# Optimization experiments

Hardware: AMD Instinct MI355X
Metric: run time of the kernel (lower is better)

## Reference

```python
import jax, jax.numpy as jnp
from jax import lax
import numpy as np

B, T = 64, 1024
N_MELS, ENC, DEC, LSTM, SPK = 80, 256, 128, 512, 256
CTX = ENC + SPK          # encoder_seq feature dim = 512
PRE = 2 * DEC            # prenet fc dims = 256
FILTERS, KS = 32, 31
MAX_R, R = 20, 1         # r buffer initialized to 1
DROP_P = 0.5


def _gru_cell(x, h, w_ih, w_hh, b_ih, b_hh):
    gi = x @ w_ih.T + b_ih
    gh = h @ w_hh.T + b_hh
    i_r, i_z, i_n = jnp.split(gi, 3, axis=-1)
    h_r, h_z, h_n = jnp.split(gh, 3, axis=-1)
    r = jax.nn.sigmoid(i_r + h_r)
    z = jax.nn.sigmoid(i_z + h_z)
    n = jnp.tanh(i_n + r * h_n)
    return (1.0 - z) * n + z * h


def _lstm_cell(x, h, c, w_ih, w_hh, b_ih, b_hh):
    g = x @ w_ih.T + h @ w_hh.T + b_ih + b_hh
    i, f, gg, o = jnp.split(g, 4, axis=-1)
    c2 = jax.nn.sigmoid(f) * c + jax.nn.sigmoid(i) * jnp.tanh(gg)
    h2 = jax.nn.sigmoid(o) * jnp.tanh(c2)
    return h2, c2


def setup_inputs() -> dict:
    key = jax.random.key(0)
    ks = jax.random.split(key, 40)
    n = lambda i, shp: jax.random.normal(ks[i], shp, jnp.float32)
    p = lambda i, shp: jax.random.normal(ks[i], shp, jnp.float32) * 0.05
    return {
        "encoder_seq": n(0, (B, T, CTX)),
        "encoder_seq_proj": n(1, (B, T, DEC)),
        "prenet_in": n(2, (B, N_MELS)),
        "attn_hidden": n(3, (B, DEC)),
        "rnn1_hidden": n(4, (B, LSTM)),
        "rnn2_hidden": n(5, (B, LSTM)),
        "rnn1_cell": n(6, (B, LSTM)),
        "rnn2_cell": n(7, (B, LSTM)),
        "context_vec": n(8, (B, CTX)),
        "chars": jax.random.randint(ks[9], (B, T), 0, 100),
        "t": 0,
        # LSA params (torch layout: Linear weight [out,in])
        "conv_w": p(10, (FILTERS, 1, KS)),
        "conv_b": p(11, (FILTERS,)),
        "L_w": p(12, (DEC, FILTERS)),
        "W_w": p(13, (DEC, DEC)),
        "W_b": p(14, (DEC,)),
        "v_w": p(15, (1, DEC)),
        # PreNet
        "fc1_w": p(16, (PRE, N_MELS)),
        "fc1_b": p(17, (PRE,)),
        "fc2_w": p(18, (PRE, PRE)),
        "fc2_b": p(19, (PRE,)),
        # GRUCell: in = CTX + PRE = 768, hidden = DEC
        "gru_w_ih": p(20, (3 * DEC, CTX + PRE)),
        "gru_w_hh": p(21, (3 * DEC, DEC)),
        "gru_b_ih": p(22, (3 * DEC,)),
        "gru_b_hh": p(23, (3 * DEC,)),
        # rnn_input Linear: CTX + DEC = 640 -> LSTM
        "ri_w": p(24, (LSTM, CTX + DEC)),
        "ri_b": p(25, (LSTM,)),
        # LSTMCells
        "l1_w_ih": p(26, (4 * LSTM, LSTM)),
        "l1_w_hh": p(27, (4 * LSTM, LSTM)),
        "l1_b_ih": p(28, (4 * LSTM,)),
        "l1_b_hh": p(29, (4 * LSTM,)),
        "l2_w_ih": p(30, (4 * LSTM, LSTM)),
        "l2_w_hh": p(31, (4 * LSTM, LSTM)),
        "l2_b_ih": p(32, (4 * LSTM,)),
        "l2_b_hh": p(33, (4 * LSTM,)),
        # output projections
        "mp_w": p(34, (N_MELS * MAX_R, LSTM)),
        "sp_w": p(35, (1, CTX + LSTM)),
        "sp_b": p(36, (1,)),
    }


def reference(encoder_seq, encoder_seq_proj, prenet_in, attn_hidden, rnn1_hidden,
              rnn2_hidden, rnn1_cell, rnn2_cell, context_vec, chars, t,
              conv_w, conv_b, L_w, W_w, W_b, v_w,
              fc1_w, fc1_b, fc2_w, fc2_b,
              gru_w_ih, gru_w_hh, gru_b_ih, gru_b_hh,
              ri_w, ri_b,
              l1_w_ih, l1_w_hh, l1_b_ih, l1_b_hh,
              l2_w_ih, l2_w_hh, l2_b_ih, l2_b_hh,
              mp_w, sp_w, sp_b):
    # PreNet (dropout always on, deterministic keys)
    dk1, dk2 = jax.random.split(jax.random.key(42))
    keep = 1.0 - DROP_P
    h = jax.nn.relu(prenet_in @ fc1_w.T + fc1_b)
    h = h * jax.random.bernoulli(dk1, keep, h.shape).astype(h.dtype) / keep
    h = jax.nn.relu(h @ fc2_w.T + fc2_b)
    prenet_out = h * jax.random.bernoulli(dk2, keep, h.shape).astype(h.dtype) / keep

    # attention GRU
    attn_h = _gru_cell(jnp.concatenate([context_vec, prenet_out], axis=-1),
                       attn_hidden, gru_w_ih, gru_w_hh, gru_b_ih, gru_b_hh)

    # LSA attention at t == 0 (cumulative attention is zeros)
    pq = attn_h @ W_w.T + W_b                              # [B, DEC]
    cumulative = jnp.zeros((B, 1, T), encoder_seq.dtype)
    loc = lax.conv_general_dilated(cumulative, conv_w, (1,), [((KS - 1) // 2,) * 2],
                                   dimension_numbers=("NCH", "OIH", "NCH"))
    loc = loc + conv_b[None, :, None]                      # [B, F, T]
    ploc = jnp.swapaxes(loc, 1, 2) @ L_w.T                 # [B, T, DEC]
    u = (jnp.tanh(pq[:, None, :] + encoder_seq_proj + ploc) @ v_w.T)[..., 0]  # [B, T]
    u = u * (chars != 0).astype(u.dtype)
    scores = jax.nn.softmax(u, axis=1)                     # [B, T]
    context = jnp.einsum("bt,btd->bd", scores, encoder_seq)  # [B, CTX]

    # residual LSTM stack (inference: no zoneout)
    x = jnp.concatenate([context, attn_h], axis=1) @ ri_w.T + ri_b
    h1, c1 = _lstm_cell(x, rnn1_hidden, rnn1_cell, l1_w_ih, l1_w_hh, l1_b_ih, l1_b_hh)
    x = x + h1
    h2, c2 = _lstm_cell(x, rnn2_hidden, rnn2_cell, l2_w_ih, l2_w_hh, l2_b_ih, l2_b_hh)
    x = x + h2

    mels = (x @ mp_w.T).reshape(B, N_MELS, MAX_R)[:, :, :R]  # [B, n_mels, r]
    stop = jax.nn.sigmoid(jnp.concatenate([x, context], axis=1) @ sp_w.T + sp_b)
    return mels, scores[:, None, :], attn_h, h1, h2, c1, c2, context, stop
```

## Files before the change

### kernel.cpp

```cpp
#include <hip/hip_runtime.h>
#include <stdint.h>

#define JAX_PARTITIONABLE 1
#define NB 512

__device__ __forceinline__ float tanh_f(float x) {
  float e = __expf(2.0f * x);
  return 1.0f - 2.0f / (e + 1.0f);
}
__device__ __forceinline__ float sigm(float x) {
  return 1.0f / (1.0f + __expf(-x));
}

__device__ __forceinline__ void stw(float* p, float v) {
  __hip_atomic_store(p, v, __ATOMIC_RELAXED, __HIP_MEMORY_SCOPE_AGENT);
}

__device__ __forceinline__ void tf2x32(unsigned k0, unsigned k1, unsigned x0, unsigned x1,
                                       unsigned &o0, unsigned &o1) {
  unsigned ks0 = k0, ks1 = k1, ks2 = k0 ^ k1 ^ 0x1BD11BDAu;
  x0 += ks0; x1 += ks1;
#define RR(r) { x0 += x1; x1 = (x1 << r) | (x1 >> (32 - r)); x1 ^= x0; }
  RR(13) RR(15) RR(26) RR(6)  x0 += ks1; x1 += ks2 + 1u;
  RR(17) RR(29) RR(16) RR(24) x0 += ks2; x1 += ks0 + 2u;
  RR(13) RR(15) RR(26) RR(6)  x0 += ks0; x1 += ks1 + 3u;
  RR(17) RR(29) RR(16) RR(24) x0 += ks1; x1 += ks2 + 4u;
  RR(13) RR(15) RR(26) RR(6)  x0 += ks2; x1 += ks0 + 5u;
#undef RR
  o0 = x0; o1 = x1;
}

__device__ __forceinline__ float drop_scale(unsigned k0, unsigned k1, unsigned flat) {
#if JAX_PARTITIONABLE
  unsigned o0, o1; tf2x32(k0, k1, 0u, flat, o0, o1);
  unsigned bits = o0 ^ o1;
#else
  unsigned o0, o1, bits;
  if (flat < 8192u) { tf2x32(k0, k1, flat, flat + 8192u, o0, o1); bits = o0; }
  else             { tf2x32(k0, k1, flat - 8192u, flat, o0, o1); bits = o1; }
#endif
  return (bits >> 31) ? 0.0f : 2.0f;
}
__device__ __forceinline__ void get_drop_keys(unsigned &a0, unsigned &a1,
                                              unsigned &b0, unsigned &b1) {
#if JAX_PARTITIONABLE
  tf2x32(0u, 42u, 0u, 0u, a0, a1);
  tf2x32(0u, 42u, 0u, 1u, b0, b1);
#else
  unsigned p0, q0, p1, q1;
  tf2x32(0u, 42u, 0u, 2u, p0, q0);
  tf2x32(0u, 42u, 1u, 3u, p1, q1);
  a0 = p0; a1 = p1; b0 = q0; b1 = q1;
#endif
}

__device__ __forceinline__ void gbar(int* ibase, int phase) {
  __syncthreads();
  if (threadIdx.x == 0) {
    const int s = (int)(blockIdx.x & 15);
    int* sub   = ibase + s * 64;
    int* top   = ibase + 1024;
    int* flags = ibase + 1088;
    int old = __hip_atomic_fetch_add(sub, 1, __ATOMIC_RELAXED, __HIP_MEMORY_SCOPE_AGENT);
    if (old == phase * 32 - 1) {
      int t = __hip_atomic_fetch_add(top, 1, __ATOMIC_RELAXED, __HIP_MEMORY_SCOPE_AGENT);
      if (t == phase * 16 - 1) {
        #pragma unroll
        for (int i = 0; i < 16; i++)
          __hip_atomic_store(flags + i * 64, phase, __ATOMIC_RELAXED, __HIP_MEMORY_SCOPE_AGENT);
      }
    }
    long long guard = 0;
    while (__hip_atomic_load(flags + s * 64, __ATOMIC_RELAXED, __HIP_MEMORY_SCOPE_AGENT) < phase) {
      __builtin_amdgcn_s_sleep(4);
      if (++guard > (1LL << 21)) break;
    }
  }
  __syncthreads();
}

__global__ void k0(int* cnt) {
  for (int i = threadIdx.x; i < 2112; i += 256) cnt[i] = 0;
}

__global__ __launch_bounds__(256, 2) void kM(
    const float* es, const float* esp, const float* prenet_in,
    const float* rnn1_hidden, const float* rnn2_hidden,
    const float* rnn1_cell, const float* rnn2_cell,
    const float* context_vec, const float* attn_hidden, const int* chars,
    const float* conv_b, const float* L_w, const float* W_w, const float* W_b, const float* v_w,
    const float* fc1_w, const float* fc1_b, const float* fc2_w, const float* fc2_b,
    const float* gru_w_ih, const float* gru_w_hh, const float* gru_b_ih, const float* gru_b_hh,
    const float* ri_w, const float* ri_b,
    const float* l1_w_ih, const float* l1_w_hh, const float* l1_b_ih, const float* l1_b_hh,
    const float* l2_w_ih, const float* l2_w_hh, const float* l2_b_ih, const float* l2_b_hh,
    const float* mp_w, const float* sp_w, const float* sp_b,
    float* ws,
    float* mels_o, float* scores_o, float* attn_o, float* h1_o, float* h2_o,
    float* c1_o, float* c2_o, float* ctx_o, float* stop_o) {
  int* ibase = (int*)ws;
  float* pqc     = ws + 2112;
  float* phT     = pqc + 128;
  float* poT     = phT + 16384;
  float* attn_hT = poT + 16384;
  float* u_buf   = attn_hT + 8192;
  float* ctxT    = u_buf + 65536;
  float* xT      = ctxT + 32768;
  float* x2T     = xT + 32768;
  float* x3T     = x2T + 32768;
  float* h1pT    = x3T + 32768;
  float* h2pT    = h1pT + 32768;
  float* cvT     = h2pT + 32768;
  float* ahT0    = cvT + 32768;
  float* c1pT    = ahT0 + 8192;
  float* c2pT    = c1pT + 32768;

  const int g = blockIdx.x, tid = threadIdx.x;
  const int w = tid >> 6, lane = tid & 63;
  __shared__ float sh[16640];

  if (g < 64) {
    for (int i = tid; i < 5120; i += 256) sh[(i / 80) * 81 + (i % 80)] = prenet_in[i];
    __syncthreads();
    unsigned d1k0, d1k1, d2k0, d2k1;
    get_drop_keys(d1k0, d1k1, d2k0, d2k1);
    const int j = g * 4 + w;
    float acc = fc1_b[j];
    const float* wr = fc1_w + j * 80;
    #pragma unroll 8
    for (int k = 0; k < 80; k += 2) {
      float2 wv = *(const float2*)(wr + k);
      acc += sh[lane * 81 + k] * wv.x + sh[lane * 81 + k + 1] * wv.y;
    }
    acc = fmaxf(acc, 0.0f) * drop_scale(d1k0, d1k1, (unsigned)(lane * 256 + j));
    stw(&phT[j * 64 + lane], acc);
  } else if (g < 128) {
    int base = (g - 64) * 512;
    #pragma unroll
    for (int e = 0; e < 2; e++) { int i = base + tid + e * 256; stw(&h1pT[i], rnn1_hidden[(i & 63) * 512 + (i >> 6)]); }
  } else if (g < 192) {
    int base = (g - 128) * 512;
    #pragma unroll
    for (int e = 0; e < 2; e++) { int i = base + tid + e * 256; stw(&h2pT[i], rnn2_hidden[(i & 63) * 512 + (i >> 6)]); }
  } else if (g < 256) {
    int base = (g - 192) * 512;
    #pragma unroll
    for (int e = 0; e < 2; e++) { int i = base + tid + e * 256; stw(&cvT[i], context_vec[(i & 63) * 512 + (i >> 6)]); }
  } else if (g < 272) {
    int base = (g - 256) * 512;
    #pragma unroll
    for (int e = 0; e < 2; e++) { int i = base + tid + e * 256; stw(&ahT0[i], attn_hidden[(i & 63) * 128 + (i >> 6)]); }
  } else if (g < 336) {
    int base = (g - 272) * 512;
    #pragma unroll
    for (int e = 0; e < 2; e++) { int i = base + tid + e * 256; stw(&c1pT[i], rnn1_cell[(i & 63) * 512 + (i >> 6)]); }
  } else if (g < 400) {
    int base = (g - 336) * 512;
    #pragma unroll
    for (int e = 0; e < 2; e++) { int i = base + tid + e * 256; stw(&c2pT[i], rnn2_cell[(i & 63) * 512 + (i >> 6)]); }
  } else if (g < 464) {
    int base = (g - 400) * 512;
    #pragma unroll
    for (int e = 0; e < 2; e++) stw(&ctxT[base + tid + e * 256], 0.0f);
  } else if (g == 464) {
    if (tid < 128) {
      float acc = W_b[tid];
      const float* lw = L_w + tid * 32;
      #pragma unroll
      for (int f = 0; f < 32; f++) acc += conv_b[f] * lw[f];
      stw(&pqc[tid], acc);
    }
  }
  gbar(ibase, 1);

  if (g < 64) {
    const int j = g * 4 + w;
    ((float4*)(sh + w * 256))[lane] = ((const float4*)(fc2_w + j * 256))[lane];
    __syncthreads();
    unsigned d1k0, d1k1, d2k0, d2k1;
    get_drop_keys(d1k0, d1k1, d2k0, d2k1);
    float acc = fc2_b[j];
    #pragma unroll 8
    for (int k = 0; k < 256; k += 2) {
      float2 wv = *(const float2*)(sh + w * 256 + k);
      acc += phT[k * 64 + lane] * wv.x + phT[(k + 1) * 64 + lane] * wv.y;
    }
    acc = fmaxf(acc, 0.0f) * drop_scale(d2k0, d2k1, (unsigned)(lane * 256 + j));
    stw(&poT[j * 64 + lane], acc);
  } else {
    const unsigned wi0 = (unsigned)((g - 64) * 256 + tid);
    float acc = 0.0f;
    #pragma unroll
    for (int s = 0; s < 10; s++) {
      unsigned idx = wi0 + (unsigned)s * 114688u;
      if (idx < 1048576u) acc += es[(size_t)idx * 32];
    }
    asm volatile("" :: "v"(acc));
  }
  gbar(ibase, 2);

  if (g < 128) {
    if (w < 3) {
      const int rj = g + 128 * w;
      const float4* src = (const float4*)(gru_w_ih + (size_t)rj * 768);
      float4* dst = (float4*)(sh + w * 768);
      #pragma unroll
      for (int q = 0; q < 3; q++) dst[q * 64 + lane] = src[q * 64 + lane];
    } else {
      float4* dst = (float4*)(sh + 2304);
      if (lane < 32) {
        dst[lane]      = ((const float4*)(gru_w_hh + (size_t)g * 128))[lane];
        dst[32 + lane] = ((const float4*)(gru_w_hh + (size_t)(128 + g) * 128))[lane];
        dst[64 + lane] = ((const float4*)(gru_w_hh + (size_t)(256 + g) * 128))[lane];
      }
    }
    __syncthreads();
    if (w < 3) {
      const int rj = g + 128 * w;
      float acc = gru_b_ih[rj];
      #pragma unroll 4
      for (int k = 0; k < 512; k += 2) {
        float2 wv = *(const float2*)(sh + w * 768 + k);
        acc += cvT[k * 64 + lane] * wv.x + cvT[(k + 1) * 64 + lane] * wv.y;
      }
      #pragma unroll 4
      for (int k = 512; k < 768; k += 2) {
        float2 wv = *(const float2*)(sh + w * 768 + k);
        acc += poT[(k - 512) * 64 + lane] * wv.x + poT[(k - 511) * 64 + lane] * wv.y;
      }
      sh[2688 + w * 64 + lane] = acc;
    } else {
      #pragma unroll
      for (int r = 0; r < 3; r++) {
        float acc = gru_b_hh[r * 128 + g];
        #pragma unroll 4
        for (int k = 0; k < 128; k += 2) {
          float2 wv = *(const float2*)(sh + 2304 + r * 128 + k);
          acc += ahT0[k * 64 + lane] * wv.x + ahT0[(k + 1) * 64 + lane] * wv.y;
        }
        sh[2688 + (3 + r) * 64 + lane] = acc;
      }
    }
    __syncthreads();
    if (tid < 64) {
      float gr = sh[2688 + tid]       + sh[2688 + 192 + tid];
      float gz = sh[2688 + 64 + tid]  + sh[2688 + 256 + tid];
      float gin = sh[2688 + 128 + tid];
      float ghn = sh[2688 + 320 + tid];
      float a0 = ahT0[g * 64 + tid];
      float r = sigm(gr), z = sigm(gz);
      float h = (1.0f - z) * tanh_f(gin + r * ghn) + z * a0;
      stw(&attn_hT[g * 64 + tid], h);
      attn_o[tid * 128 + g] = h;
    }
  } else {
    const unsigned wi0 = (unsigned)((g - 128) * 256 + tid);
    float acc = 0.0f;
    #pragma unroll
    for (int s = 0; s < 3; s++) {
      unsigned idx = wi0 + (unsigned)s * 98304u;
      if (idx < 262144u) acc += esp[(size_t)idx * 32];
    }
    if (g == 128) { if (tid < 512) acc += W_w[tid * 32]; }
    if (g == 129) {
      #pragma unroll
      for (int s = 0; s < 8; s++) acc += (float)chars[(tid + s * 256) * 32];
    }
    asm volatile("" :: "v"(acc));
  }
  gbar(ibase, 3);

  {
    const int b = g >> 3, tch = g & 7;
    {
      const float4* src = (const float4*)(W_w + (size_t)(w * 32) * 128);
      float4* dst = (float4*)(sh + w * 4096);
      #pragma unroll
      for (int q = 0; q < 16; q++) dst[q * 64 + lane] = src[q * 64 + lane];
    }
    float* pqs = sh + 16384;
    float* shh = sh + 16512;
    if (tid < 128) shh[tid] = attn_hT[tid * 64 + b];
    __syncthreads();
    float2 a2; a2.x = shh[2 * lane]; a2.y = shh[2 * lane + 1];
    for (int ni = 0; ni < 32; ni++) {
      int n = w * 32 + ni;
      float2 wv2 = *(const float2*)(sh + w * 4096 + ni * 128 + 2 * lane);
      float s = a2.x * wv2.x + a2.y * wv2.y;
      for (int off = 32; off > 0; off >>= 1) s += __shfl_xor(s, off, 64);
      if (lane == 0) pqs[n] = s + pqc[n];
    }
    __syncthreads();
    float2 p = *(const float2*)(pqs + 2 * lane);
    float2 v2 = *(const float2*)(v_w + 2 * lane);
    const int tb = tch * 128 + w * 32;
    const float* erow = esp + ((size_t)b * 1024 + tb) * 128 + 2 * lane;
    for (int i2 = 0; i2 < 8; i2++) {
      const float* er = erow + (size_t)i2 * 512;
      float2 e0 = *(const float2*)(er);
      float2 e1 = *(const float2*)(er + 128);
      float2 e2 = *(const float2*)(er + 256);
      float2 e3 = *(const float2*)(er + 384);
      float s0 = v2.x * tanh_f(p.x + e0.x) + v2.y * tanh_f(p.y + e0.y);
      float s1 = v2.x * tanh_f(p.x + e1.x) + v2.y * tanh_f(p.y + e1.y);
      float s2 = v2.x * tanh_f(p.x + e2.x) + v2.y * tanh_f(p.y + e2.y);
      float s3 = v2.x * tanh_f(p.x + e3.x) + v2.y * tanh_f(p.y + e3.y);
      for (int off = 32; off > 0; off >>= 1) {
        s0 += __shfl_down(s0, off, 64);
        s1 += __shfl_down(s1, off, 64);
        s2 += __shfl_down(s2, off, 64);
        s3 += __shfl_down(s3, off, 64);
      }
      if (lane == 0) {
        int t = tb + i2 * 4;
        stw(&u_buf[b * 1024 + t],     (chars[b * 1024 + t]     != 0) ? s0 : 0.0f);
        stw(&u_buf[b * 1024 + t + 1], (chars[b * 1024 + t + 1] != 0) ? s1 : 0.0f);
        stw(&u_buf[b * 1024 + t + 2], (chars[b * 1024 + t + 2] != 0) ? s2 : 0.0f);
        stw(&u_buf[b * 1024 + t + 3], (chars[b * 1024 + t + 3] != 0) ? s3 : 0.0f);
      }
    }
  }
  gbar(ibase, 4);

  {
    const int b = g >> 3, tch = g & 7;
    float* redm = sh;
    float* sc   = sh + 256;
    float* red4 = sh + 384;
    float4 uv = *(const float4*)(u_buf + b * 1024 + tid * 4);
    float m = fmaxf(fmaxf(uv.x, uv.y), fmaxf(uv.z, uv.w));
    redm[tid] = m;
    __syncthreads();
    for (int s = 128; s > 0; s >>= 1) { if (tid < s) redm[tid] = fmaxf(redm[tid], redm[tid + s]); __syncthreads(); }
    float M = redm[0];
    __syncthreads();
    float e0 = __expf(uv.x - M), e1 = __expf(uv.y - M), e2 = __expf(uv.z - M), e3 = __expf(uv.w - M);
    redm[tid] = e0 + e1 + e2 + e3;
    __syncthreads();
    for (int s = 128; s > 0; s >>= 1) { if (tid < s) redm[tid] += redm[tid + s]; __syncthreads(); }
    float inv = 1.0f / redm[0];
    if (tch == 0) {
      float4 r; r.x = e0 * inv; r.y = e1 * inv; r.z = e2 * inv; r.w = e3 * inv;
      *(float4*)(scores_o + b * 1024 + tid * 4) = r;
    }
    if (tid < 128) sc[tid] = __expf(u_buf[b * 1024 + tch * 128 + tid] - M) * inv;
    __syncthreads();
    float acc0 = 0, acc1 = 0, acc2 = 0, acc3 = 0, acc4 = 0, acc5 = 0, acc6 = 0, acc7 = 0;
    const float* base = es + ((size_t)b * 1024 + tch * 128) * 512 + lane * 8;
    for (int i = 0; i < 32; i += 2) {
      int t1 = 4 * i + w, t2 = t1 + 4;
      float4 wa1 = *(const float4*)(base + (size_t)t1 * 512);
      float4 wb1 = *(const float4*)(base + (size_t)t1 * 512 + 4);
      float4 wa2 = *(const float4*)(base + (size_t)t2 * 512);
      float4 wb2 = *(const float4*)(base + (size_t)t2 * 512 + 4);
      float s1 = sc[t1], s2 = sc[t2];
      acc0 += s1 * wa1.x + s2 * wa2.x; acc1 += s1 * wa1.y + s2 * wa2.y;
      acc2 += s1 * wa1.z + s2 * wa2.z; acc3 += s1 * wa1.w + s2 * wa2.w;
      acc4 += s1 * wb1.x + s2 * wb2.x; acc5 += s1 * wb1.y + s2 * wb2.y;
      acc6 += s1 * wb1.z + s2 * wb2.z; acc7 += s1 * wb1.w + s2 * wb2.w;
    }
    float* rr = red4 + w * 512 + lane * 8;
    rr[0] = acc0; rr[1] = acc1; rr[2] = acc2; rr[3] = acc3;
    rr[4] = acc4; rr[5] = acc5; rr[6] = acc6; rr[7] = acc7;
    __syncthreads();
    int d0 = tid * 2;
    float r0 = red4[d0] + red4[512 + d0] + red4[1024 + d0] + red4[1536 + d0];
    float r1 = red4[d0 + 1] + red4[512 + d0 + 1] + red4[1024 + d0 + 1] + red4[1536 + d0 + 1];
    atomicAdd(&ctxT[d0 * 64 + b], r0);
    atomicAdd(&ctxT[(d0 + 1) * 64 + b], r1);
  }
  gbar(ibase, 5);

  {
    const int n = g;
    if (tid < 160) ((float4*)sh)[tid] = ((const float4*)(ri_w + (size_t)n * 640))[tid];
    if (tid < 64) ctx_o[tid * 512 + n] = ctxT[n * 64 + tid];
    __syncthreads();
    const int k0 = w * 160;
    float acc = 0.0f;
    for (int k = k0; k < k0 + 160; k += 2) {
      float2 wv2 = *(const float2*)(sh + k);
      float x0 = (k < 512) ? ctxT[k * 64 + lane] : attn_hT[(k - 512) * 64 + lane];
      float x1 = (k + 1 < 512) ? ctxT[(k + 1) * 64 + lane] : attn_hT[(k - 511) * 64 + lane];
      acc += x0 * wv2.x + x1 * wv2.y;
    }
    sh[640 + w * 64 + lane] = acc;
    __syncthreads();
    if (tid < 64) stw(&xT[n * 64 + tid], ri_b[n] + sh[640 + tid] + sh[704 + tid] + sh[768 + tid] + sh[832 + tid]);
  }
  gbar(ibase, 6);

  {
    const int n = g + (w << 9);
    {
      const float4* si = (const float4*)(l1_w_ih + (size_t)n * 512);
      const float4* sh4 = (const float4*)(l1_w_hh + (size_t)n * 512);
      float4* di = (float4*)(sh + w * 1024);
      float4* dh = (float4*)(sh + w * 1024 + 512);
      #pragma unroll
      for (int q = 0; q < 2; q++) { di[q * 64 + lane] = si[q * 64 + lane]; dh[q * 64 + lane] = sh4[q * 64 + lane]; }
    }
    __syncthreads();
    float acc = l1_b_ih[n] + l1_b_hh[n];
    #pragma unroll 4
    for (int k = 0; k < 512; k += 2) {
      float2 wv2 = *(const float2*)(sh + w * 1024 + k);
      acc += xT[k * 64 + lane] * wv2.x + xT[(k + 1) * 64 + lane] * wv2.y;
    }
    #pragma unroll 4
    for (int k = 0; k < 512; k += 2) {
      float2 wv2 = *(const float2*)(sh + w * 1024 + 512 + k);
      acc += h1pT[k * 64 + lane] * wv2.x + h1pT[(k + 1) * 64 + lane] * wv2.y;
    }
    sh[4096 + w * 64 + lane] = acc;
    __syncthreads();
    if (tid < 64) {
      float gi = sh[4096 + tid], gf = sh[4160 + tid], gg = sh[4224 + tid], go = sh[4288 + tid];
      float c = c1pT[g * 64 + tid];
      float c2 = sigm(gf) * c + sigm(gi) * tanh_f(gg);
      float h2v = sigm(go) * tanh_f(c2);
      h1_o[tid * 512 + g] = h2v;
      c1_o[tid * 512 + g] = c2;
      stw(&x2T[g * 64 + tid], xT[g * 64 + tid] + h2v);
    }
  }
  gbar(ibase, 7);

  {
    const int n = g + (w << 9);
    {
      const float4* si = (const float4*)(l2_w_ih + (size_t)n * 512);
      const float4* sh4 = (const float4*)(l2_w_hh + (size_t)n * 512);
      float4* di = (float4*)(sh + w * 1024);
      float4* dh = (float4*)(sh + w * 1024 + 512);
      #pragma unroll
      for (int q = 0; q < 2; q++) { di[q * 64 + lane] = si[q * 64 + lane]; dh[q * 64 + lane] = sh4[q * 64 + lane]; }
    }
    __syncthreads();
    float acc = l2_b_ih[n] + l2_b_hh[n];
    #pragma unroll 4
    for (int k = 0; k < 512; k += 2) {
      float2 wv2 = *(const float2*)(sh + w * 1024 + k);
      acc += x2T[k * 64 + lane] * wv2.x + x2T[(k + 1) * 64 + lane] * wv2.y;
    }
    #pragma unroll 4
    for (int k = 0; k < 512; k += 2) {
      float2 wv2 = *(const float2*)(sh + w * 1024 + 512 + k);
      acc += h2pT[k * 64 + lane] * wv2.x + h2pT[(k + 1) * 64 + lane] * wv2.y;
    }
    sh[4096 + w * 64 + lane] = acc;
    __syncthreads();
    if (tid < 64) {
      float gi = sh[4096 + tid], gf = sh[4160 + tid], gg = sh[4224 + tid], go = sh[4288 + tid];
      float c = c2pT[g * 64 + tid];
      float c2 = sigm(gf) * c + sigm(gi) * tanh_f(gg);
      float h2v = sigm(go) * tanh_f(c2);
      h2_o[tid * 512 + g] = h2v;
      c2_o[tid * 512 + g] = c2;
      stw(&x3T[g * 64 + tid], x2T[g * 64 + tid] + h2v);
    }
  }
  gbar(ibase, 8);

  if (g < 20) {
    #pragma unroll
    for (int q = 0; q < 2; q++) {
      int idx = q * 256 + tid;
      int j = idx >> 7, c = idx & 127;
      ((float4*)sh)[idx] = ((const float4*)(mp_w + (size_t)(g * 4 + j) * 20 * 512))[c];
    }
    __syncthreads();
    float acc0 = 0, acc1 = 0, acc2 = 0, acc3 = 0;
    for (int kk = 0; kk < 128; kk++) {
      int k = w * 128 + kk;
      float x3 = x3T[k * 64 + lane];
      acc0 += x3 * sh[k]; acc1 += x3 * sh[512 + k]; acc2 += x3 * sh[1024 + k]; acc3 += x3 * sh[1536 + k];
    }
    sh[2048 + w * 256 + 0 * 64 + lane] = acc0;
    sh[2048 + w * 256 + 1 * 64 + lane] = acc1;
    sh[2048 + w * 256 + 2 * 64 + lane] = acc2;
    sh[2048 + w * 256 + 3 * 64 + lane] = acc3;
    __syncthreads();
    int j = tid >> 6, ln = tid & 63;
    float s = sh[2048 + j * 64 + ln] + sh[2304 + j * 64 + ln] + sh[2560 + j * 64 + ln] + sh[2816 + j * 64 + ln];
    mels_o[ln * 80 + g * 4 + j] = s;
  } else if (g == 20) {
    ((float4*)sh)[tid] = ((const float4*)sp_w)[tid];
    __syncthreads();
    float acc = 0;
    for (int kk = 0; kk < 128; kk++) {
      int k = w * 128 + kk;
      acc += x3T[k * 64 + lane] * sh[k] + ctxT[k * 64 + lane] * sh[512 + k];
    }
    sh[1024 + w * 64 + lane] = acc;
    __syncthreads();
    if (tid < 64) stop_o[tid] = sigm(sp_b[0] + sh[1024 + tid] + sh[1088 + tid] + sh[1152 + tid] + sh[1216 + tid]);
  }
}

extern "C" void kernel_launch(void* const* d_in, const int* in_sizes, int n_in,
                              void* d_out, int out_size, void* d_ws, size_t ws_size,
                              hipStream_t stream) {
  const float* es          = (const float*)d_in[0];
  const float* esp         = (const float*)d_in[1];
  const float* prenet_in   = (const float*)d_in[2];
  const float* attn_hidden = (const float*)d_in[3];
  const float* rnn1_hidden = (const float*)d_in[4];
  const float* rnn2_hidden = (const float*)d_in[5];
  const float* rnn1_cell   = (const float*)d_in[6];
  const float* rnn2_cell   = (const float*)d_in[7];
  const float* context_vec = (const float*)d_in[8];
  const int* chars         = (const int*)d_in[9];
  const float* conv_b = (const float*)d_in[12];
  const float* L_w    = (const float*)d_in[13];
  const float* W_w    = (const float*)d_in[14];
  const float* W_b    = (const float*)d_in[15];
  const float* v_w    = (const float*)d_in[16];
  const float* fc1_w  = (const float*)d_in[17];
  const float* fc1_b  = (const float*)d_in[18];
  const float* fc2_w  = (const float*)d_in[19];
  const float* fc2_b  = (const float*)d_in[20];
  const float* gru_w_ih = (const float*)d_in[21];
  const float* gru_w_hh = (const float*)d_in[22];
  const float* gru_b_ih = (const float*)d_in[23];
  const float* gru_b_hh = (const float*)d_in[24];
  const float* ri_w   = (const float*)d_in[25];
  const float* ri_b   = (const float*)d_in[26];
  const float* l1_w_ih = (const float*)d_in[27];
  const float* l1_w_hh = (const float*)d_in[28];
  const float* l1_b_ih = (const float*)d_in[29];
  const float* l1_b_hh = (const float*)d_in[30];
  const float* l2_w_ih = (const float*)d_in[31];
  const float* l2_w_hh = (const float*)d_in[32];
  const float* l2_b_ih = (const float*)d_in[33];
  const float* l2_b_hh = (const float*)d_in[34];
  const float* mp_w = (const float*)d_in[35];
  const float* sp_w = (const float*)d_in[36];
  const float* sp_b = (const float*)d_in[37];

  float* out = (float*)d_out;
  float* ws = (float*)d_ws;

  float* mels_o   = out + 0;
  float* scores_o = out + 5120;
  float* attn_o   = out + 70656;
  float* h1_o     = out + 78848;
  float* h2_o     = out + 111616;
  float* c1_o     = out + 144384;
  float* c2_o     = out + 177152;
  float* ctx_o    = out + 209920;
  float* stop_o   = out + 242688;

  k0<<<1, 256, 0, stream>>>((int*)ws);
  kM<<<NB, 256, 0, stream>>>(es, esp, prenet_in, rnn1_hidden, rnn2_hidden,
                             rnn1_cell, rnn2_cell, context_vec, attn_hidden, chars,
                             conv_b, L_w, W_w, W_b, v_w,
                             fc1_w, fc1_b, fc2_w, fc2_b,
                             gru_w_ih, gru_w_hh, gru_b_ih, gru_b_hh,
                             ri_w, ri_b,
                             l1_w_ih, l1_w_hh, l1_b_ih, l1_b_hh,
                             l2_w_ih, l2_w_hh, l2_b_ih, l2_b_hh,
                             mp_w, sp_w, sp_b,
                             ws,
                             mels_o, scores_o, attn_o, h1_o, h2_o,
                             c1_o, c2_o, ctx_o, stop_o);
}
```

Baseline: 487.3 us.

## Switch inter-stage activation buffers to k-quad interleaved layout for float4 loads

```diff
diff --git a/kernel.cpp b/kernel.cpp
--- a/kernel.cpp
+++ b/kernel.cpp
@@ -14,6 +14,12 @@
 
 __device__ __forceinline__ void stw(float* p, float v) {
   __hip_atomic_store(p, v, __ATOMIC_RELAXED, __HIP_MEMORY_SCOPE_AGENT);
+}
+__device__ __forceinline__ void stw4(float* p, float4 v) {
+  union { float2 f; uint64_t u; } a, b;
+  a.f.x = v.x; a.f.y = v.y; b.f.x = v.z; b.f.y = v.w;
+  __hip_atomic_store((uint64_t*)p, a.u, __ATOMIC_RELAXED, __HIP_MEMORY_SCOPE_AGENT);
+  __hip_atomic_store(((uint64_t*)p) + 1, b.u, __ATOMIC_RELAXED, __HIP_MEMORY_SCOPE_AGENT);
 }
 
 __device__ __forceinline__ void tf2x32(unsigned k0, unsigned k1, unsigned x0, unsigned x1,
@@ -99,21 +105,33 @@
     float* mels_o, float* scores_o, float* attn_o, float* h1_o, float* h2_o,
     float* c1_o, float* c2_o, float* ctx_o, float* stop_o) {
   int* ibase = (int*)ws;
-  float* pqc     = ws + 2112;
-  float* phT     = pqc + 128;
-  float* poT     = phT + 16384;
-  float* attn_hT = poT + 16384;
-  float* u_buf   = attn_hT + 8192;
-  float* ctxT    = u_buf + 65536;
-  float* xT      = ctxT + 32768;
-  float* x2T     = xT + 32768;
-  float* x3T     = x2T + 32768;
-  float* h1pT    = x3T + 32768;
-  float* h2pT    = h1pT + 32768;
-  float* cvT     = h2pT + 32768;
-  float* ahT0    = cvT + 32768;
-  float* c1pT    = ahT0 + 8192;
-  float* c2pT    = c1pT + 32768;
+  float* pqc    = ws + 2112;
+  float* phq    = ws + 2240;
+  float* poq    = ws + 18624;
+  float* ahq_h  = ws + 35008;
+  float* u_buf  = ws + 43200;
+  float* ctxq   = ws + 108736;
+  float* xq     = ws + 141504;
+  float* x2q    = ws + 174272;
+  float* x3q    = ws + 207040;
+  float* hq1    = ws + 239808;
+  float* hq2    = ws + 272576;
+  float* cvq    = ws + 305344;
+  float* ahq_in = ws + 338112;
+  float* c1pT   = ws + 346304;
+  float* c2pT   = ws + 379072;
+
+  const float4* cvq4   = (const float4*)cvq;
+  const float4* phq4   = (const float4*)phq;
+  const float4* poq4   = (const float4*)poq;
+  const float4* ahq_in4= (const float4*)ahq_in;
+  const float4* ahq_h4 = (const float4*)ahq_h;
+  const float4* ctxq4  = (const float4*)ctxq;
+  const float4* xq4    = (const float4*)xq;
+  const float4* x2q4   = (const float4*)x2q;
+  const float4* x3q4   = (const float4*)x3q;
+  const float4* hq14   = (const float4*)hq1;
+  const float4* hq24   = (const float4*)hq2;
 
   const int g = blockIdx.x, tid = threadIdx.x;
   const int w = tid >> 6, lane = tid & 63;
@@ -133,36 +151,36 @@
       acc += sh[lane * 81 + k] * wv.x + sh[lane * 81 + k + 1] * wv.y;
     }
     acc = fmaxf(acc, 0.0f) * drop_scale(d1k0, d1k1, (unsigned)(lane * 256 + j));
-    stw(&phT[j * 64 + lane], acc);
+    stw(&phq[g * 256 + lane * 4 + w], acc);
+  } else if (g < 96) {
+    int t = (g - 64) * 256 + tid;
+    int k4 = t >> 6, b = t & 63;
+    stw4(&hq1[k4 * 256 + b * 4], ((const float4*)rnn1_hidden)[b * 128 + k4]);
   } else if (g < 128) {
-    int base = (g - 64) * 512;
-    #pragma unroll
-    for (int e = 0; e < 2; e++) { int i = base + tid + e * 256; stw(&h1pT[i], rnn1_hidden[(i & 63) * 512 + (i >> 6)]); }
-  } else if (g < 192) {
-    int base = (g - 128) * 512;
-    #pragma unroll
-    for (int e = 0; e < 2; e++) { int i = base + tid + e * 256; stw(&h2pT[i], rnn2_hidden[(i & 63) * 512 + (i >> 6)]); }
-  } else if (g < 256) {
-    int base = (g - 192) * 512;
-    #pragma unroll
-    for (int e = 0; e < 2; e++) { int i = base + tid + e * 256; stw(&cvT[i], context_vec[(i & 63) * 512 + (i >> 6)]); }
-  } else if (g < 272) {
-    int base = (g - 256) * 512;
-    #pragma unroll
-    for (int e = 0; e < 2; e++) { int i = base + tid + e * 256; stw(&ahT0[i], attn_hidden[(i & 63) * 128 + (i >> 6)]); }
-  } else if (g < 336) {
-    int base = (g - 272) * 512;
+    int t = (g - 96) * 256 + tid;
+    int k4 = t >> 6, b = t & 63;
+    stw4(&hq2[k4 * 256 + b * 4], ((const float4*)rnn2_hidden)[b * 128 + k4]);
+  } else if (g < 160) {
+    int t = (g - 128) * 256 + tid;
+    int k4 = t >> 6, b = t & 63;
+    stw4(&cvq[k4 * 256 + b * 4], ((const float4*)context_vec)[b * 128 + k4]);
+  } else if (g < 168) {
+    int t = (g - 160) * 256 + tid;
+    int k4 = t >> 6, b = t & 63;
+    stw4(&ahq_in[k4 * 256 + b * 4], ((const float4*)attn_hidden)[b * 32 + k4]);
+  } else if (g < 232) {
+    int base = (g - 168) * 512;
     #pragma unroll
     for (int e = 0; e < 2; e++) { int i = base + tid + e * 256; stw(&c1pT[i], rnn1_cell[(i & 63) * 512 + (i >> 6)]); }
-  } else if (g < 400) {
-    int base = (g - 336) * 512;
+  } else if (g < 296) {
+    int base = (g - 232) * 512;
     #pragma unroll
     for (int e = 0; e < 2; e++) { int i = base + tid + e * 256; stw(&c2pT[i], rnn2_cell[(i & 63) * 512 + (i >> 6)]); }
-  } else if (g < 464) {
-    int base = (g - 400) * 512;
+  } else if (g < 360) {
+    int base = (g - 296) * 512;
     #pragma unroll
-    for (int e = 0; e < 2; e++) stw(&ctxT[base + tid + e * 256], 0.0f);
-  } else if (g == 464) {
+    for (int e = 0; e < 2; e++) stw(&ctxq[base + tid + e * 256], 0.0f);
+  } else if (g == 360) {
     if (tid < 128) {
       float acc = W_b[tid];
       const float* lw = L_w + tid * 32;
@@ -170,6 +188,12 @@
       for (int f = 0; f < 32; f++) acc += conv_b[f] * lw[f];
       stw(&pqc[tid], acc);
     }
+  } else {
+    const unsigned wi0 = (unsigned)((g - 361) * 256 + tid);
+    float acc = 0.0f;
+    #pragma unroll
+    for (int s = 0; s < 10; s++) acc += es[(size_t)(wi0 + (unsigned)s * 38656u) * 32];
+    asm volatile("" :: "v"(acc));
   }
   gbar(ibase, 1);
 
@@ -179,20 +203,22 @@
     __syncthreads();
     unsigned d1k0, d1k1, d2k0, d2k1;
     get_drop_keys(d1k0, d1k1, d2k0, d2k1);
+    const float4* wv4 = (const float4*)(sh + w * 256);
     float acc = fc2_b[j];
     #pragma unroll 8
-    for (int k = 0; k < 256; k += 2) {
-      float2 wv = *(const float2*)(sh + w * 256 + k);
-      acc += phT[k * 64 + lane] * wv.x + phT[(k + 1) * 64 + lane] * wv.y;
+    for (int k4 = 0; k4 < 64; k4++) {
+      float4 x4 = phq4[k4 * 64 + lane];
+      float4 wv = wv4[k4];
+      acc += x4.x * wv.x + x4.y * wv.y + x4.z * wv.z + x4.w * wv.w;
     }
     acc = fmaxf(acc, 0.0f) * drop_scale(d2k0, d2k1, (unsigned)(lane * 256 + j));
-    stw(&poT[j * 64 + lane], acc);
+    stw(&poq[g * 256 + lane * 4 + w], acc);
   } else {
     const unsigned wi0 = (unsigned)((g - 64) * 256 + tid);
     float acc = 0.0f;
     #pragma unroll
-    for (int s = 0; s < 10; s++) {
-      unsigned idx = wi0 + (unsigned)s * 114688u;
+    for (int s = 0; s < 6; s++) {
+      unsigned idx = 386560u + wi0 + (unsigned)s * 114688u;
       if (idx < 1048576u) acc += es[(size_t)idx * 32];
     }
     asm volatile("" :: "v"(acc));
@@ -209,34 +235,39 @@
     } else {
       float4* dst = (float4*)(sh + 2304);
       if (lane < 32) {
-        dst[lane]      = ((const float4*)(gru_w_hh + (size_t)g * 128))[lane];
-        dst[32 + lane] = ((const float4*)(gru_w_hh + (size_t)(128 + g) * 128))[lane];
-        dst[64 + lane] = ((const float4*)(gru_w_hh + (size_t)(256 + g) * 128))[lane];
+        dst[lane]      = ((const float4*)gru_w_hh)[(size_t)g * 32 + lane];
+        dst[32 + lane] = ((const float4*)gru_w_hh)[(size_t)(128 + g) * 32 + lane];
+        dst[64 + lane] = ((const float4*)gru_w_hh)[(size_t)(256 + g) * 32 + lane];
       }
     }
     __syncthreads();
     if (w < 3) {
       const int rj = g + 128 * w;
+      const float4* wv4 = (const float4*)(sh + w * 768);
       float acc = gru_b_ih[rj];
       #pragma unroll 4
-      for (int k = 0; k < 512; k += 2) {
-        float2 wv = *(const float2*)(sh + w * 768 + k);
-        acc += cvT[k * 64 + lane] * wv.x + cvT[(k + 1) * 64 + lane] * wv.y;
+      for (int k4 = 0; k4 < 128; k4++) {
+        float4 x4 = cvq4[k4 * 64 + lane];
+        float4 wv = wv4[k4];
+        acc += x4.x * wv.x + x4.y * wv.y + x4.z * wv.z + x4.w * wv.w;
       }
       #pragma unroll 4
-      for (int k = 512; k < 768; k += 2) {
-        float2 wv = *(const float2*)(sh + w * 768 + k);
-        acc += poT[(k - 512) * 64 + lane] * wv.x + poT[(k - 511) * 64 + lane] * wv.y;
+      for (int k4 = 0; k4 < 64; k4++) {
+        float4 x4 = poq4[k4 * 64 + lane];
+        float4 wv = wv4[128 + k4];
+        acc += x4.x * wv.x + x4.y * wv.y + x4.z * wv.z + x4.w * wv.w;
       }
       sh[2688 + w * 64 + lane] = acc;
     } else {
+      const float4* wh4 = (const float4*)(sh + 2304);
       #pragma unroll
       for (int r = 0; r < 3; r++) {
         float acc = gru_b_hh[r * 128 + g];
         #pragma unroll 4
-        for (int k = 0; k < 128; k += 2) {
-          float2 wv = *(const float2*)(sh + 2304 + r * 128 + k);
-          acc += ahT0[k * 64 + lane] * wv.x + ahT0[(k + 1) * 64 + lane] * wv.y;
+        for (int k4 = 0; k4 < 32; k4++) {
+          float4 x4 = ahq_in4[k4 * 64 + lane];
+          float4 wv = wh4[r * 32 + k4];
+          acc += x4.x * wv.x + x4.y * wv.y + x4.z * wv.z + x4.w * wv.w;
         }
         sh[2688 + (3 + r) * 64 + lane] = acc;
       }
@@ -247,10 +278,10 @@
       float gz = sh[2688 + 64 + tid]  + sh[2688 + 256 + tid];
       float gin = sh[2688 + 128 + tid];
       float ghn = sh[2688 + 320 + tid];
-      float a0 = ahT0[g * 64 + tid];
+      float a0 = ahq_in[(g >> 2) * 256 + tid * 4 + (g & 3)];
       float r = sigm(gr), z = sigm(gz);
       float h = (1.0f - z) * tanh_f(gin + r * ghn) + z * a0;
-      stw(&attn_hT[g * 64 + tid], h);
+      stw(&ahq_h[(g >> 2) * 256 + tid * 4 + (g & 3)], h);
       attn_o[tid * 128 + g] = h;
     }
   } else {
@@ -273,14 +304,14 @@
   {
     const int b = g >> 3, tch = g & 7;
     {
-      const float4* src = (const float4*)(W_w + (size_t)(w * 32) * 128);
-      float4* dst = (float4*)(sh + w * 4096);
+      const float4* src = ((const float4*)W_w) + (size_t)(w * 32) * 32;
+      float4* dst = (float4*)sh + w * 1024;
       #pragma unroll
       for (int q = 0; q < 16; q++) dst[q * 64 + lane] = src[q * 64 + lane];
     }
     float* pqs = sh + 16384;
     float* shh = sh + 16512;
-    if (tid < 128) shh[tid] = attn_hT[tid * 64 + b];
+    if (tid < 128) shh[tid] = ahq_h[(tid >> 2) * 256 + b * 4 + (tid & 3)];
     __syncthreads();
     float2 a2; a2.x = shh[2 * lane]; a2.y = shh[2 * lane + 1];
     for (int ni = 0; ni < 32; ni++) {
@@ -366,27 +397,26 @@
     int d0 = tid * 2;
     float r0 = red4[d0] + red4[512 + d0] + red4[1024 + d0] + red4[1536 + d0];
     float r1 = red4[d0 + 1] + red4[512 + d0 + 1] + red4[1024 + d0 + 1] + red4[1536 + d0 + 1];
-    atomicAdd(&ctxT[d0 * 64 + b], r0);
-    atomicAdd(&ctxT[(d0 + 1) * 64 + b], r1);
+    atomicAdd(&ctxq[(d0 >> 2) * 256 + b * 4 + (d0 & 3)], r0);
+    atomicAdd(&ctxq[((d0 + 1) >> 2) * 256 + b * 4 + ((d0 + 1) & 3)], r1);
   }
   gbar(ibase, 5);
 
   {
     const int n = g;
     if (tid < 160) ((float4*)sh)[tid] = ((const float4*)(ri_w + (size_t)n * 640))[tid];
-    if (tid < 64) ctx_o[tid * 512 + n] = ctxT[n * 64 + tid];
-    __syncthreads();
-    const int k0 = w * 160;
+    if (tid < 64) ctx_o[tid * 512 + n] = ctxq[(n >> 2) * 256 + tid * 4 + (n & 3)];
+    __syncthreads();
     float acc = 0.0f;
-    for (int k = k0; k < k0 + 160; k += 2) {
-      float2 wv2 = *(const float2*)(sh + k);
-      float x0 = (k < 512) ? ctxT[k * 64 + lane] : attn_hT[(k - 512) * 64 + lane];
-      float x1 = (k + 1 < 512) ? ctxT[(k + 1) * 64 + lane] : attn_hT[(k - 511) * 64 + lane];
-      acc += x0 * wv2.x + x1 * wv2.y;
+    for (int k4 = w * 40; k4 < w * 40 + 40; k4++) {
+      float4 wv = ((float4*)sh)[k4];
+      float4 x4 = (k4 < 128) ? ctxq4[k4 * 64 + lane] : ahq_h4[(k4 - 128) * 64 + lane];
+      acc += x4.x * wv.x + x4.y * wv.y + x4.z * wv.z + x4.w * wv.w;
     }
     sh[640 + w * 64 + lane] = acc;
     __syncthreads();
-    if (tid < 64) stw(&xT[n * 64 + tid], ri_b[n] + sh[640 + tid] + sh[704 + tid] + sh[768 + tid] + sh[832 + tid]);
+    if (tid < 64) stw(&xq[(n >> 2) * 256 + tid * 4 + (n & 3)],
+                      ri_b[n] + sh[640 + tid] + sh[704 + tid] + sh[768 + tid] + sh[832 + tid]);
   }
   gbar(ibase, 6);
 
@@ -395,22 +425,26 @@
     {
       const float4* si = (const float4*)(l1_w_ih + (size_t)n * 512);
       const float4* sh4 = (const float4*)(l1_w_hh + (size_t)n * 512);
-      float4* di = (float4*)(sh + w * 1024);
-      float4* dh = (float4*)(sh + w * 1024 + 512);
+      float4* di = (float4*)sh + w * 256;
+      float4* dh = di + 128;
       #pragma unroll
       for (int q = 0; q < 2; q++) { di[q * 64 + lane] = si[q * 64 + lane]; dh[q * 64 + lane] = sh4[q * 64 + lane]; }
     }
     __syncthreads();
+    const float4* di = (const float4*)sh + w * 256;
+    const float4* dh = di + 128;
     float acc = l1_b_ih[n] + l1_b_hh[n];
     #pragma unroll 4
-    for (int k = 0; k < 512; k += 2) {
-      float2 wv2 = *(const float2*)(sh + w * 1024 + k);
-      acc += xT[k * 64 + lane] * wv2.x + xT[(k + 1) * 64 + lane] * wv2.y;
+    for (int k4 = 0; k4 < 128; k4++) {
+      float4 x4 = xq4[k4 * 64 + lane];
+      float4 wv = di[k4];
+      acc += x4.x * wv.x + x4.y * wv.y + x4.z * wv.z + x4.w * wv.w;
     }
     #pragma unroll 4
-    for (int k = 0; k < 512; k += 2) {
-      float2 wv2 = *(const float2*)(sh + w * 1024 + 512 + k);
-      acc += h1pT[k * 64 + lane] * wv2.x + h1pT[(k + 1) * 64 + lane] * wv2.y;
+    for (int k4 = 0; k4 < 128; k4++) {
+      float4 x4 = hq14[k4 * 64 + lane];
+      float4 wv = dh[k4];
+      acc += x4.x * wv.x + x4.y * wv.y + x4.z * wv.z + x4.w * wv.w;
     }
     sh[4096 + w * 64 + lane] = acc;
     __syncthreads();
@@ -421,7 +455,8 @@
       float h2v = sigm(go) * tanh_f(c2);
       h1_o[tid * 512 + g] = h2v;
       c1_o[tid * 512 + g] = c2;
-      stw(&x2T[g * 64 + tid], xT[g * 64 + tid] + h2v);
+      stw(&x2q[(g >> 2) * 256 + tid * 4 + (g & 3)],
+          xq[(g >> 2) * 256 + tid * 4 + (g & 3)] + h2v);
     }
   }
   gbar(ibase, 7);
@@ -431,22 +466,26 @@
     {
       const float4* si = (const float4*)(l2_w_ih + (size_t)n * 512);
       const float4* sh4 = (const float4*)(l2_w_hh + (size_t)n * 512);
-      float4* di = (float4*)(sh + w * 1024);
-      float4* dh = (float4*)(sh + w * 1024 + 512);
+      float4* di = (float4*)sh + w * 256;
+      float4* dh = di + 128;
       #pragma unroll
       for (int q = 0; q < 2; q++) { di[q * 64 + lane] = si[q * 64 + lane]; dh[q * 64 + lane] = sh4[q * 64 + lane]; }
     }
     __syncthreads();
+    const float4* di = (const float4*)sh + w * 256;
+    const float4* dh = di + 128;
     float acc = l2_b_ih[n] + l2_b_hh[n];
     #pragma unroll 4
-    for (int k = 0; k < 512; k += 2) {
-      float2 wv2 = *(const float2*)(sh + w * 1024 + k);
-      acc += x2T[k * 64 + lane] * wv2.x + x2T[(k + 1) * 64 + lane] * wv2.y;
+    for (int k4 = 0; k4 < 128; k4++) {
+      float4 x4 = x2q4[k4 * 64 + lane];
+      float4 wv = di[k4];
+      acc += x4.x * wv.x + x4.y * wv.y + x4.z * wv.z + x4.w * wv.w;
     }
     #pragma unroll 4
-    for (int k = 0; k < 512; k += 2) {
-      float2 wv2 = *(const float2*)(sh + w * 1024 + 512 + k);
-      acc += h2pT[k * 64 + lane] * wv2.x + h2pT[(k + 1) * 64 + lane] * wv2.y;
+    for (int k4 = 0; k4 < 128; k4++) {
+      float4 x4 = hq24[k4 * 64 + lane];
+      float4 wv = dh[k4];
+      acc += x4.x * wv.x + x4.y * wv.y + x4.z * wv.z + x4.w * wv.w;
     }
     sh[4096 + w * 64 + lane] = acc;
     __syncthreads();
@@ -457,40 +496,36 @@
       float h2v = sigm(go) * tanh_f(c2);
       h2_o[tid * 512 + g] = h2v;
       c2_o[tid * 512 + g] = c2;
-      stw(&x3T[g * 64 + tid], x2T[g * 64 + tid] + h2v);
+      stw(&x3q[(g >> 2) * 256 + tid * 4 + (g & 3)],
+          x2q[(g >> 2) * 256 + tid * 4 + (g & 3)] + h2v);
     }
   }
   gbar(ibase, 8);
 
-  if (g < 20) {
-    #pragma unroll
-    for (int q = 0; q < 2; q++) {
-      int idx = q * 256 + tid;
-      int j = idx >> 7, c = idx & 127;
-      ((float4*)sh)[idx] = ((const float4*)(mp_w + (size_t)(g * 4 + j) * 20 * 512))[c];
-    }
-    __syncthreads();
-    float acc0 = 0, acc1 = 0, acc2 = 0, acc3 = 0;
-    for (int kk = 0; kk < 128; kk++) {
-      int k = w * 128 + kk;
-      float x3 = x3T[k * 64 + lane];
-      acc0 += x3 * sh[k]; acc1 += x3 * sh[512 + k]; acc2 += x3 * sh[1024 + k]; acc3 += x3 * sh[1536 + k];
-    }
-    sh[2048 + w * 256 + 0 * 64 + lane] = acc0;
-    sh[2048 + w * 256 + 1 * 64 + lane] = acc1;
-    sh[2048 + w * 256 + 2 * 64 + lane] = acc2;
-    sh[2048 + w * 256 + 3 * 64 + lane] = acc3;
-    __syncthreads();
-    int j = tid >> 6, ln = tid & 63;
-    float s = sh[2048 + j * 64 + ln] + sh[2304 + j * 64 + ln] + sh[2560 + j * 64 + ln] + sh[2816 + j * 64 + ln];
-    mels_o[ln * 80 + g * 4 + j] = s;
-  } else if (g == 20) {
+  if (g < 80) {
+    const int m = g;
+    if (tid < 128) ((float4*)sh)[tid] = ((const float4*)(mp_w + (size_t)m * 20 * 512))[tid];
+    __syncthreads();
+    float acc = 0.0f;
+    for (int k4 = w * 32; k4 < w * 32 + 32; k4++) {
+      float4 x4 = x3q4[k4 * 64 + lane];
+      float4 wv = ((float4*)sh)[k4];
+      acc += x4.x * wv.x + x4.y * wv.y + x4.z * wv.z + x4.w * wv.w;
+    }
+    sh[512 + w * 64 + lane] = acc;
+    __syncthreads();
+    if (tid < 64) mels_o[tid * 80 + m] = sh[512 + tid] + sh[576 + tid] + sh[640 + tid] + sh[704 + tid];
+  } else if (g == 80) {
     ((float4*)sh)[tid] = ((const float4*)sp_w)[tid];
     __syncthreads();
-    float acc = 0;
-    for (int kk = 0; kk < 128; kk++) {
-      int k = w * 128 + kk;
-      acc += x3T[k * 64 + lane] * sh[k] + ctxT[k * 64 + lane] * sh[512 + k];
+    float acc = 0.0f;
+    for (int k4 = w * 32; k4 < w * 32 + 32; k4++) {
+      float4 x4 = x3q4[k4 * 64 + lane];
+      float4 c4 = ctxq4[k4 * 64 + lane];
+      float4 w1 = ((float4*)sh)[k4];
+      float4 w2 = ((float4*)sh)[128 + k4];
+      acc += x4.x * w1.x + x4.y * w1.y + x4.z * w1.z + x4.w * w1.w;
+      acc += c4.x * w2.x + c4.y * w2.y + c4.z * w2.z + c4.w * w2.w;
     }
     sh[1024 + w * 64 + lane] = acc;
     __syncthreads();
```

Measured after the change: 425.6 us. 1.15x faster.
